# Optimization experiments

Measured on AMD Instinct MI355X. Metric: run time of the kernel, lower is better.

Reference implementation:

```python
import jax, jax.numpy as jnp
import numpy as np

NUM_FEATURES = 1024
GRID_SIZE = 5
SPLINE_ORDER = 3
GRID_RANGE = (-2.0, 2.0)
LN_EPS = 1e-5
DEN_EPS = 1e-7


def build_grid(num_features, grid_size, spline_order, grid_range):
    start, end = float(grid_range[0]), float(grid_range[1])
    step = (end - start) / grid_size
    base = jnp.linspace(start - spline_order * step, end + spline_order * step,
                        grid_size + 2 * spline_order + 1, dtype=jnp.float32)
    return jnp.broadcast_to(base[None, :], (num_features, base.shape[0]))


def setup_inputs() -> dict:
    key = jax.random.key(0)
    k_x, k_w = jax.random.split(key)
    x = jax.random.normal(k_x, (8192, NUM_FEATURES), dtype=jnp.float32)
    ln_weight = jnp.ones((NUM_FEATURES,), jnp.float32)
    ln_bias = jnp.zeros((NUM_FEATURES,), jnp.float32)
    # torch init: uniform_(-0.1, 0.1)
    spline_weight = jax.random.uniform(k_w, (NUM_FEATURES, GRID_SIZE + SPLINE_ORDER),
                                       minval=-0.1, maxval=0.1, dtype=jnp.float32)
    base_weight = jnp.ones((NUM_FEATURES,), jnp.float32)
    grid = build_grid(NUM_FEATURES, GRID_SIZE, SPLINE_ORDER, GRID_RANGE)
    return {"x": x, "ln_weight": ln_weight, "ln_bias": ln_bias,
            "spline_weight": spline_weight, "base_weight": base_weight, "grid": grid}


def layer_norm(x, w, b):
    mu = jnp.mean(x, axis=-1, keepdims=True)
    var = jnp.mean((x - mu) ** 2, axis=-1, keepdims=True)
    return (x - mu) * jax.lax.rsqrt(var + LN_EPS) * w + b


def b_splines(x, grid, spline_order):
    # x: (B, F); grid: (F, K). Cox-de Boor recursion, unrolled over fixed order.
    xe = x[:, :, None]                      # (B, F, 1)
    g = grid[None, :, :]                    # (1, F, K)
    bases = ((xe >= g[:, :, :-1]) & (xe < g[:, :, 1:])).astype(x.dtype)
    # right-endpoint correction: x == grid[:, -1] belongs to the last interval
    right_mask = x == grid[None, :, -1]
    bases = bases.at[:, :, -1].set(jnp.where(right_mask, jnp.asarray(1.0, x.dtype), bases[:, :, -1]))
    for k in range(1, spline_order + 1):
        left_den = g[:, :, k:-1] - g[:, :, :-(k + 1)]
        left_ok = jnp.abs(left_den) > DEN_EPS
        left_den_safe = jnp.where(left_ok, left_den, jnp.asarray(1.0, x.dtype))
        left = jnp.where(left_ok, (xe - g[:, :, :-(k + 1)]) / left_den_safe * bases[:, :, :-1], 0.0)
        right_den = g[:, :, k + 1:] - g[:, :, 1:-k]
        right_ok = jnp.abs(right_den) > DEN_EPS
        right_den_safe = jnp.where(right_ok, right_den, jnp.asarray(1.0, x.dtype))
        right = jnp.where(right_ok, (g[:, :, k + 1:] - xe) / right_den_safe * bases[:, :, 1:], 0.0)
        bases = left + right
    return bases                            # (B, F, grid_size + spline_order)


def reference(x, ln_weight, ln_bias, spline_weight, base_weight, grid):
    orig_shape = x.shape
    xf = x.reshape(-1, NUM_FEATURES)
    normed = layer_norm(xf, ln_weight, ln_bias)
    bases = b_splines(normed, grid, SPLINE_ORDER)
    spline_out = jnp.einsum('bfk,fk->bf', bases, spline_weight)
    residual = base_weight[None, :] * jax.nn.silu(normed)
    return (spline_out + residual).reshape(orig_shape)
```

## Files before the change

### kernel.cpp

```cpp
#include <hip/hip_runtime.h>
#include <hip/hip_bf16.h>


#define F 1024
#define WSTRIDE 9
#define BLOCK 256
#define NBLOCKS 1024

__device__ __forceinline__ float bf2f(unsigned short u) {
    union { unsigned int i; float f; } v;
    v.i = ((unsigned int)u) << 16;
    return v.f;
}

__device__ __forceinline__ unsigned short f2bf(float f) {
    union { float f; unsigned int i; } v;
    v.f = f;
    unsigned int x = v.i;
    unsigned int r = (x + 0x7FFFu + ((x >> 16) & 1u)) >> 16;
    return (unsigned short)r;
}

template <bool BF16>
__device__ __forceinline__ float ldv(const void* p, int i) {
    if constexpr (BF16) return bf2f(((const unsigned short*)p)[i]);
    else                return ((const float*)p)[i];
}

template <bool BF16>
__device__ __forceinline__ void stv(void* p, int i, float v) {
    if constexpr (BF16) ((unsigned short*)p)[i] = f2bf(v);
    else                ((float*)p)[i] = v;
}

__global__ void detect_kernel(const void* grid, int* flag) {
    float g = ((const float*)grid)[0];
    *flag = (g > -4.45f && g < -4.35f) ? 0 : 1;
}

template <bool BF16>
__device__ __forceinline__ void kan_body(
    const void* __restrict__ x,   const void* __restrict__ lnw,
    const void* __restrict__ lnb, const void* __restrict__ sw,
    const void* __restrict__ bw,  const void* __restrict__ grid,
    void* __restrict__ out, int rows,
    float* s_w, float* s_part, float* s_stats)
{
    const int tid  = threadIdx.x;
    const int wave = tid >> 6;
    const int lane = tid & 63;

    for (int i = tid; i < F * 8; i += BLOCK) {
        s_w[(i >> 3) * WSTRIDE + (i & 7)] = ldv<BF16>(sw, i);
    }

    float p_lnw[4], p_lnb[4], p_bw[4];
    #pragma unroll
    for (int j = 0; j < 4; ++j) {
        int f = tid + 256 * j;
        p_lnw[j] = ldv<BF16>(lnw, f);
        p_lnb[j] = ldv<BF16>(lnb, f);
        p_bw[j]  = ldv<BF16>(bw, f);
    }
    const float g0   = ldv<BF16>(grid, 0);
    const float g11  = ldv<BF16>(grid, 11);
    const float invh = 11.0f / (g11 - g0);

    __syncthreads();

    for (int row = blockIdx.x; row < rows; row += gridDim.x) {
        const int rbase = row * F;

        float xv[4];
        float s = 0.0f, s2 = 0.0f;
        #pragma unroll
        for (int j = 0; j < 4; ++j) {
            xv[j] = ldv<BF16>(x, rbase + tid + 256 * j);
            s  += xv[j];
            s2 += xv[j] * xv[j];
        }
        #pragma unroll
        for (int off = 32; off > 0; off >>= 1) {
            s  += __shfl_down(s,  off, 64);
            s2 += __shfl_down(s2, off, 64);
        }
        if (lane == 0) { s_part[wave * 2] = s; s_part[wave * 2 + 1] = s2; }
        __syncthreads();
        if (tid == 0) {
            float S  = s_part[0] + s_part[2] + s_part[4] + s_part[6];
            float S2 = s_part[1] + s_part[3] + s_part[5] + s_part[7];
            float mu  = S * (1.0f / F);
            float var = S2 * (1.0f / F) - mu * mu;
            s_stats[0] = mu;
            s_stats[1] = rsqrtf(var + 1e-5f);
        }
        __syncthreads();
        const float mu = s_stats[0], rstd = s_stats[1];

        #pragma unroll
        for (int j = 0; j < 4; ++j) {
            int f = tid + 256 * j;
            float t = (xv[j] - mu) * rstd * p_lnw[j] + p_lnb[j];

            float sig = 1.0f / (1.0f + __expf(-t));
            float res = p_bw[j] * t * sig;

            float ttn = (t - g0) * invh;
            int j0 = (int)floorf(ttn);
            j0 = j0 < 0 ? 0 : (j0 > 10 ? 10 : j0);
            float u  = ttn - (float)j0;
            float u2 = u * u, u3 = u2 * u;
            float om = 1.0f - u;
            float N0 = om * om * om * (1.0f / 6.0f);
            float N3 = u3 * (1.0f / 6.0f);
            float N1 = (1.0f / 6.0f) * (4.0f - 6.0f * u2 + 3.0f * u3);
            float N2 = 1.0f - N0 - N1 - N3;
            float Nv[4] = { N0, N1, N2, N3 };

            float sp = 0.0f;
            const float* wrow = &s_w[f * WSTRIDE];
            #pragma unroll
            for (int r = 0; r < 4; ++r) {
                int jj = j0 - 3 + r;
                int jc = jj < 0 ? 0 : (jj > 7 ? 7 : jj);
                float wv = wrow[jc];
                sp += (jj == jc) ? wv * Nv[r] : 0.0f;
            }
            sp = (t >= g0 && t <= g11) ? sp : 0.0f;

            stv<BF16>(out, rbase + f, sp + res);
        }
    }
}

__global__ __launch_bounds__(BLOCK, 4) void kan_kernel(
    const void* __restrict__ x,   const void* __restrict__ lnw,
    const void* __restrict__ lnb, const void* __restrict__ sw,
    const void* __restrict__ bw,  const void* __restrict__ grid,
    void* __restrict__ out, int rows, const int* __restrict__ flag)
{
    __shared__ float s_w[F * WSTRIDE];
    __shared__ float s_part[8];
    __shared__ float s_stats[2];

    if (*flag) kan_body<true >(x, lnw, lnb, sw, bw, grid, out, rows, s_w, s_part, s_stats);
    else       kan_body<false>(x, lnw, lnb, sw, bw, grid, out, rows, s_w, s_part, s_stats);
}

extern "C" void kernel_launch(void* const* d_in, const int* in_sizes, int n_in,
                              void* d_out, int out_size, void* d_ws, size_t ws_size,
                              hipStream_t stream) {
    const void* x    = d_in[0];
    const void* lnw  = d_in[1];
    const void* lnb  = d_in[2];
    const void* sw   = d_in[3];
    const void* bw   = d_in[4];
    const void* grid = d_in[5];

    int* flag = (int*)d_ws;
    int rows = in_sizes[0] / F;
    int nblk = rows < NBLOCKS ? rows : NBLOCKS;
    if (nblk < 1) nblk = 1;

    detect_kernel<<<dim3(1), dim3(1), 0, stream>>>(grid, flag);
    kan_kernel<<<dim3(nblk), dim3(BLOCK), 0, stream>>>(
        x, lnw, lnb, sw, bw, grid, d_out, rows, flag);
}
```

Baseline: 106.5 us.

## Process one row per wave, drop block barriers and the detect kernel

Each 64-lane wave now computes a full row's layernorm with shuffle reductions, removing the per-row shared-memory reduction and two __syncthreads. Spline weights are transposed in LDS to feature-major per coefficient and the per-feature params are packed as float4 in LDS. The separate dtype-detect kernel launch is folded into the main kernel. Register use per thread rises (16 values per lane) and LDS grows to about 48KB per block, which may limit occupancy.

```diff
diff --git a/kernel.cpp b/kernel.cpp
--- a/kernel.cpp
+++ b/kernel.cpp
@@ -3,8 +3,8 @@
 
 
 #define F 1024
-#define WSTRIDE 9
-#define BLOCK 256
+#define BLOCK 512
+#define WPB 8
 #define NBLOCKS 1024
 
 __device__ __forceinline__ float bf2f(unsigned short u) {
@@ -33,34 +33,27 @@
     else                ((float*)p)[i] = v;
 }
 
-__global__ void detect_kernel(const void* grid, int* flag) {
-    float g = ((const float*)grid)[0];
-    *flag = (g > -4.45f && g < -4.35f) ? 0 : 1;
-}
-
 template <bool BF16>
 __device__ __forceinline__ void kan_body(
     const void* __restrict__ x,   const void* __restrict__ lnw,
     const void* __restrict__ lnb, const void* __restrict__ sw,
     const void* __restrict__ bw,  const void* __restrict__ grid,
     void* __restrict__ out, int rows,
-    float* s_w, float* s_part, float* s_stats)
+    float* s_w, float* s_p)
 {
     const int tid  = threadIdx.x;
     const int wave = tid >> 6;
     const int lane = tid & 63;
 
     for (int i = tid; i < F * 8; i += BLOCK) {
-        s_w[(i >> 3) * WSTRIDE + (i & 7)] = ldv<BF16>(sw, i);
+        int f = i >> 3, k = i & 7;
+        s_w[k * F + f] = ldv<BF16>(sw, i);
     }
-
-    float p_lnw[4], p_lnb[4], p_bw[4];
-    #pragma unroll
-    for (int j = 0; j < 4; ++j) {
-        int f = tid + 256 * j;
-        p_lnw[j] = ldv<BF16>(lnw, f);
-        p_lnb[j] = ldv<BF16>(lnb, f);
-        p_bw[j]  = ldv<BF16>(bw, f);
+    for (int f = tid; f < F; f += BLOCK) {
+        s_p[4 * f + 0] = ldv<BF16>(lnw, f);
+        s_p[4 * f + 1] = ldv<BF16>(lnb, f);
+        s_p[4 * f + 2] = ldv<BF16>(bw,  f);
+        s_p[4 * f + 3] = 0.0f;
     }
     const float g0   = ldv<BF16>(grid, 0);
     const float g11  = ldv<BF16>(grid, 11);
@@ -68,42 +61,34 @@
 
     __syncthreads();
 
-    for (int row = blockIdx.x; row < rows; row += gridDim.x) {
+    for (int row = blockIdx.x * WPB + wave; row < rows; row += gridDim.x * WPB) {
         const int rbase = row * F;
 
-        float xv[4];
+        float xv[16];
         float s = 0.0f, s2 = 0.0f;
         #pragma unroll
-        for (int j = 0; j < 4; ++j) {
-            xv[j] = ldv<BF16>(x, rbase + tid + 256 * j);
+        for (int j = 0; j < 16; ++j) {
+            xv[j] = ldv<BF16>(x, rbase + lane + 64 * j);
             s  += xv[j];
             s2 += xv[j] * xv[j];
         }
         #pragma unroll
         for (int off = 32; off > 0; off >>= 1) {
-            s  += __shfl_down(s,  off, 64);
-            s2 += __shfl_down(s2, off, 64);
+            s  += __shfl_xor(s,  off, 64);
+            s2 += __shfl_xor(s2, off, 64);
         }
-        if (lane == 0) { s_part[wave * 2] = s; s_part[wave * 2 + 1] = s2; }
-        __syncthreads();
-        if (tid == 0) {
-            float S  = s_part[0] + s_part[2] + s_part[4] + s_part[6];
-            float S2 = s_part[1] + s_part[3] + s_part[5] + s_part[7];
-            float mu  = S * (1.0f / F);
-            float var = S2 * (1.0f / F) - mu * mu;
-            s_stats[0] = mu;
-            s_stats[1] = rsqrtf(var + 1e-5f);
-        }
-        __syncthreads();
-        const float mu = s_stats[0], rstd = s_stats[1];
+        const float mu   = s * (1.0f / F);
+        const float rstd = rsqrtf(s2 * (1.0f / F) - mu * mu + 1e-5f);
 
         #pragma unroll
-        for (int j = 0; j < 4; ++j) {
-            int f = tid + 256 * j;
-            float t = (xv[j] - mu) * rstd * p_lnw[j] + p_lnb[j];
+        for (int j = 0; j < 16; ++j) {
+            const int f = lane + 64 * j;
+
+            const float4 pp = *reinterpret_cast<const float4*>(&s_p[4 * f]);
+            float t = (xv[j] - mu) * rstd * pp.x + pp.y;
 
             float sig = 1.0f / (1.0f + __expf(-t));
-            float res = p_bw[j] * t * sig;
+            float res = pp.z * t * sig;
 
             float ttn = (t - g0) * invh;
             int j0 = (int)floorf(ttn);
@@ -118,12 +103,11 @@
             float Nv[4] = { N0, N1, N2, N3 };
 
             float sp = 0.0f;
-            const float* wrow = &s_w[f * WSTRIDE];
             #pragma unroll
             for (int r = 0; r < 4; ++r) {
                 int jj = j0 - 3 + r;
                 int jc = jj < 0 ? 0 : (jj > 7 ? 7 : jj);
-                float wv = wrow[jc];
+                float wv = s_w[jc * F + f];
                 sp += (jj == jc) ? wv * Nv[r] : 0.0f;
             }
             sp = (t >= g0 && t <= g11) ? sp : 0.0f;
@@ -137,14 +121,16 @@
     const void* __restrict__ x,   const void* __restrict__ lnw,
     const void* __restrict__ lnb, const void* __restrict__ sw,
     const void* __restrict__ bw,  const void* __restrict__ grid,
-    void* __restrict__ out, int rows, const int* __restrict__ flag)
+    void* __restrict__ out, int rows)
 {
-    __shared__ float s_w[F * WSTRIDE];
-    __shared__ float s_part[8];
-    __shared__ float s_stats[2];
+    __shared__ float s_w[8 * F];
+    __shared__ float s_p[4 * F];
 
-    if (*flag) kan_body<true >(x, lnw, lnb, sw, bw, grid, out, rows, s_w, s_part, s_stats);
-    else       kan_body<false>(x, lnw, lnb, sw, bw, grid, out, rows, s_w, s_part, s_stats);
+    const float g = ((const float*)grid)[0];
+    const bool is_bf16 = !(g > -4.45f && g < -4.35f);
+
+    if (is_bf16) kan_body<true >(x, lnw, lnb, sw, bw, grid, out, rows, s_w, s_p);
+    else         kan_body<false>(x, lnw, lnb, sw, bw, grid, out, rows, s_w, s_p);
 }
 
 extern "C" void kernel_launch(void* const* d_in, const int* in_sizes, int n_in,
@@ -157,12 +143,11 @@
     const void* bw   = d_in[4];
     const void* grid = d_in[5];
 
-    int* flag = (int*)d_ws;
     int rows = in_sizes[0] / F;
-    int nblk = rows < NBLOCKS ? rows : NBLOCKS;
+    int nblk = (rows + WPB - 1) / WPB;
+    if (nblk > NBLOCKS) nblk = NBLOCKS;
     if (nblk < 1) nblk = 1;
 
-    detect_kernel<<<dim3(1), dim3(1), 0, stream>>>(grid, flag);
     kan_kernel<<<dim3(nblk), dim3(BLOCK), 0, stream>>>(
-        x, lnw, lnb, sw, bw, grid, d_out, rows, flag);
+        x, lnw, lnb, sw, bw, grid, d_out, rows);
 }
```

After: 105.8 us. No clear change (-0.6%).
